# Kernel tuning notes

Measured on AMD Instinct MI355X. Metric: run time of the kernel, lower is better.

The kernel has to match this reference:

```python
import jax, jax.numpy as jnp
import numpy as np

NUM_HEADS = 8
LN_EPS = 1e-5


def layer_norm(x, g, b):
    m = jnp.mean(x, axis=-1, keepdims=True)
    v = jnp.mean((x - m) ** 2, axis=-1, keepdims=True)
    return (x - m) * jax.lax.rsqrt(v + LN_EPS) * g + b


def setup_inputs() -> dict:
    key = jax.random.key(0)
    B, Nq, Nk, D = 4, 2048, 2048, 256
    F = 4 * D
    ks = jax.random.split(key, 12)
    s = 0.02
    inp = {
        "q": jax.random.normal(ks[0], (B, Nq, D), jnp.float32),
        "x": jax.random.normal(ks[1], (B, Nk, D), jnp.float32),
        "Wq": jax.random.normal(ks[2], (D, D), jnp.float32) * s,
        "bq": jnp.zeros((D,), jnp.float32),
        "Wk": jax.random.normal(ks[3], (D, D), jnp.float32) * s,
        "bk": jnp.zeros((D,), jnp.float32),
        "Wv": jax.random.normal(ks[4], (D, D), jnp.float32) * s,
        "bv": jnp.zeros((D,), jnp.float32),
        "Wo": jax.random.normal(ks[5], (D, D), jnp.float32) * s,
        "bo": jnp.zeros((D,), jnp.float32),
        "Wm": jax.random.normal(ks[6], (D, F), jnp.float32) * s,
        "bm": jnp.zeros((F,), jnp.float32),
        "We": jax.random.normal(ks[7], (F, D), jnp.float32) * s,
        "be": jnp.zeros((D,), jnp.float32),
        "g0": jnp.ones((D,), jnp.float32),
        "b0": jnp.zeros((D,), jnp.float32),
        "g1": jnp.ones((D,), jnp.float32),
        "b1": jnp.zeros((D,), jnp.float32),
    }
    return inp


def reference(q, x, Wq, bq, Wk, bk, Wv, bv, Wo, bo, Wm, bm, We, be, g0, b0, g1, b1):
    B, Nq, D = q.shape
    H = NUM_HEADS
    dh = D // H
    scale = 1.0 / np.sqrt(dh).astype(np.float32)
    # projections, split into heads (split(dim_split,2)+cat(.,0) == head reshape)
    Q = (q @ Wq + bq).reshape(B, Nq, H, dh)
    K = (x @ Wk + bk).reshape(B, -1, H, dh)
    V = (x @ Wv + bv).reshape(B, -1, H, dh)
    A = jax.nn.softmax(jnp.einsum("bqhd,bkhd->bhqk", Q, K) * scale, axis=-1)
    # residual on the projected query (Q_ + A @ V_), merge heads
    O = (Q + jnp.einsum("bhqk,bkhd->bqhd", A, V)).reshape(B, Nq, D)
    O = layer_norm(O, g0, b0)
    O = O + jax.nn.relu(O @ Wo + bo)
    identity = O
    O = layer_norm(O, g1, b1)  # dropout p=0.0 is identity
    O = jax.nn.relu(O @ Wm + bm) @ We + be
    return O + identity
```

## Files before the change

kernel.cpp:

```cpp
#include <hip/hip_runtime.h>
#include <math.h>
#include <stdint.h>

typedef __attribute__((ext_vector_type(8))) __bf16 bf16x8;
typedef __attribute__((ext_vector_type(16))) float f32x16;

#define Z16 {0.f,0.f,0.f,0.f,0.f,0.f,0.f,0.f,0.f,0.f,0.f,0.f,0.f,0.f,0.f,0.f}

__device__ __forceinline__ unsigned short f2b(float f) {
  union { float f; uint32_t u; } v; v.f = f;
  uint32_t r = (v.u + 0x7FFFu + ((v.u >> 16) & 1u)) >> 16;
  return (unsigned short)r;
}
__device__ __forceinline__ float b2f(unsigned short u) {
  union { uint32_t u; float f; } v; v.u = ((uint32_t)u) << 16;
  return v.f;
}
__device__ __forceinline__ uint32_t pk2(float a, float b) {
  return (uint32_t)f2b(a) | ((uint32_t)f2b(b) << 16);
}
__device__ __forceinline__ uint32_t cvtpk(float lo, float hi) {
  uint32_t r;
  asm("v_cvt_pk_bf16_f32 %0, %1, %2" : "=v"(r) : "v"(lo), "v"(hi));
  return r;
}
__device__ __forceinline__ void glds16(const void* g, void* l) {
  __builtin_amdgcn_global_load_lds(
      (const __attribute__((address_space(1))) void*)g,
      (__attribute__((address_space(3))) void*)l, 16, 0, 0);
}
#define MFMA32(a, b, c) __builtin_amdgcn_mfma_f32_32x32x16_bf16(a, b, c, 0, 0, 0)

__global__ __launch_bounds__(256) void prep(
    const float* __restrict__ q, const float* __restrict__ x,
    unsigned short* __restrict__ qh, unsigned short* __restrict__ xh,
    const float* __restrict__ Wq, const float* __restrict__ Wk,
    const float* __restrict__ Wv, const float* __restrict__ Wo,
    const float* __restrict__ Wm, const float* __restrict__ We,
    unsigned short* __restrict__ WqT, unsigned short* __restrict__ WkvT,
    unsigned short* __restrict__ WoT, unsigned short* __restrict__ WmT,
    unsigned short* __restrict__ WeT,
    const float* __restrict__ bk, const float* __restrict__ bv,
    float* __restrict__ bkv) {
  __shared__ float T[64][68];
  const int bx = blockIdx.x, tid = threadIdx.x;
  if (bx < 2048) {
    const float* src = (bx < 1024) ? q : x;
    unsigned short* dst = (bx < 1024) ? qh : xh;
    const int i = (bx & 1023) * 256 + tid;
    float4 a = ((const float4*)src)[i * 2];
    float4 b = ((const float4*)src)[i * 2 + 1];
    uint4 o;
    o.x = cvtpk(a.x, a.y); o.y = cvtpk(a.z, a.w);
    o.z = cvtpk(b.x, b.y); o.w = cvtpk(b.z, b.w);
    ((uint4*)dst)[i] = o;
  } else if (bx < 2240) {
    int t = bx - 2048;
    const float* in; unsigned short* out; int ldin, ldout, kx, nx;
    if (t < 16)       { in = Wq; out = WqT;           ldin = 256;  ldout = 256;  kx = t & 3;  nx = t >> 2; }
    else if (t < 32)  { t -= 16;  in = Wk; out = WkvT;          ldin = 256;  ldout = 256;  kx = t & 3;  nx = t >> 2; }
    else if (t < 48)  { t -= 32;  in = Wv; out = WkvT + 65536;  ldin = 256;  ldout = 256;  kx = t & 3;  nx = t >> 2; }
    else if (t < 64)  { t -= 48;  in = Wo; out = WoT;           ldin = 256;  ldout = 256;  kx = t & 3;  nx = t >> 2; }
    else if (t < 128) { t -= 64;  in = Wm; out = WmT;           ldin = 1024; ldout = 256;  kx = t & 3;  nx = t >> 2; }
    else              { t -= 128; in = We; out = WeT;           ldin = 256;  ldout = 1024; kx = t & 15; nx = t >> 4; }
    const int k0 = kx * 64, n0 = nx * 64;
    const int r = tid >> 2, c16 = (tid & 3) * 16;
    #pragma unroll
    for (int i = 0; i < 4; ++i)
      *(float4*)&T[r][c16 + i * 4] =
          *(const float4*)&in[(size_t)(k0 + r) * ldin + n0 + c16 + i * 4];
    __syncthreads();
    const int n = tid >> 2, k16 = (tid & 3) * 16;
    uint32_t wb[8];
    #pragma unroll
    for (int p = 0; p < 8; ++p)
      wb[p] = cvtpk(T[k16 + 2 * p][n], T[k16 + 2 * p + 1][n]);
    uint4 o0, o1;
    o0.x = wb[0]; o0.y = wb[1]; o0.z = wb[2]; o0.w = wb[3];
    o1.x = wb[4]; o1.y = wb[5]; o1.z = wb[6]; o1.w = wb[7];
    *(uint4*)&out[(size_t)(n0 + n) * ldout + k0 + k16] = o0;
    *(uint4*)&out[(size_t)(n0 + n) * ldout + k0 + k16 + 8] = o1;
  } else {
    if (tid < 256) { bkv[tid] = bk[tid]; bkv[256 + tid] = bv[tid]; }
  }
}

__global__ __launch_bounds__(256, 2) void gemm_kv(
    const unsigned short* __restrict__ A, int lda,
    const unsigned short* __restrict__ Bt, int ldb,
    const float* __restrict__ bias,
    unsigned short* __restrict__ VtOut,
    void* __restrict__ Cout, int ldc, int K) {
  __shared__ __align__(16) unsigned short As[2 * 128 * 64];
  __shared__ __align__(16) unsigned short Bs[2 * 64 * 64];
  const int tid = threadIdx.x, lane = tid & 63, wid = tid >> 6;
  const int l31 = lane & 31, g2 = lane >> 5;
  const int m0 = blockIdx.x * 128, n0 = blockIdx.y * 64;

  const char* srcA[4];
  const char* srcB[2];
  #pragma unroll
  for (int p = 0; p < 4; ++p) {
    int row = p * 32 + wid * 8 + (lane >> 3);
    srcA[p] = (const char*)A + ((size_t)(m0 + row) * lda) * 2 + (lane & 7) * 16;
  }
  #pragma unroll
  for (int p = 0; p < 2; ++p) {
    int row = p * 32 + wid * 8 + (lane >> 3);
    srcB[p] = (const char*)Bt + ((size_t)(n0 + row) * ldb) * 2 + (lane & 7) * 16;
  }

  f32x16 acc0 = Z16, acc1 = Z16;
  const int nt = K >> 6;

  #pragma unroll
  for (int p = 0; p < 4; ++p) { glds16(srcA[p], &As[p * 2048 + wid * 512]); srcA[p] += 128; }
  #pragma unroll
  for (int p = 0; p < 2; ++p) { glds16(srcB[p], &Bs[p * 2048 + wid * 512]); srcB[p] += 128; }
  __syncthreads();

  for (int t = 0; t < nt; ++t) {
    const int cur = t & 1, nxt = cur ^ 1;
    if (t + 1 < nt) {
      #pragma unroll
      for (int p = 0; p < 4; ++p) { glds16(srcA[p], &As[nxt * 8192 + p * 2048 + wid * 512]); srcA[p] += 128; }
      #pragma unroll
      for (int p = 0; p < 2; ++p) { glds16(srcB[p], &Bs[nxt * 4096 + p * 2048 + wid * 512]); srcB[p] += 128; }
    }
    const char* as = (const char*)As + cur * 16384;
    const char* bs = (const char*)Bs + cur * 8192;
    #pragma unroll
    for (int kc = 0; kc < 4; ++kc) {
      const int xo = kc * 32 + g2 * 16;
      bf16x8 af  = *(const bf16x8*)(as + (wid * 32 + l31) * 128 + xo);
      bf16x8 b0v = *(const bf16x8*)(bs + l31 * 128 + xo);
      bf16x8 b1v = *(const bf16x8*)(bs + (32 + l31) * 128 + xo);
      acc0 = MFMA32(af, b0v, acc0);
      acc1 = MFMA32(af, b1v, acc1);
    }
    __syncthreads();
  }

  const int bb = m0 >> 11;
  #pragma unroll
  for (int nb = 0; nb < 2; ++nb) {
    const f32x16& acc = nb ? acc1 : acc0;
    const int col = n0 + nb * 32 + l31;
    const float bs = bias[col];
    if (n0 < 256) {
      #pragma unroll
      for (int r = 0; r < 16; ++r) {
        const int m = m0 + wid * 32 + (r & 3) + 8 * (r >> 2) + 4 * g2;
        ((unsigned short*)Cout)[(size_t)m * ldc + col] = f2b(acc[r] + bs);
      }
    } else {
      const int hv = (col - 256) >> 5, dv = (col - 256) & 31;
      unsigned short* vrow = VtOut + ((size_t)(bb * 8 + hv) * 32 + dv) * 2048;
      #pragma unroll
      for (int tq = 0; tq < 4; ++tq) {
        const int ks = (m0 & 2047) + wid * 32 + 8 * tq + 4 * g2;
        uint2 wv;
        wv.x = pk2(acc[4 * tq + 0] + bs, acc[4 * tq + 1] + bs);
        wv.y = pk2(acc[4 * tq + 2] + bs, acc[4 * tq + 3] + bs);
        *(uint2*)(vrow + ks) = wv;
      }
    }
  }
}

template <int EPI>
__global__ __launch_bounds__(256, 2) void gemm_small(
    const unsigned short* __restrict__ A, int lda,
    const unsigned short* __restrict__ Bt, int ldb,
    const float* __restrict__ bias,
    const unsigned short* __restrict__ res, int ldr,
    void* __restrict__ Cout, int ldc, int K) {
  __shared__ __align__(16) unsigned short As[2 * 64 * 64];
  __shared__ __align__(16) unsigned short Bs[2 * 64 * 64];
  const int tid = threadIdx.x, lane = tid & 63, wid = tid >> 6;
  const int l31 = lane & 31, g2 = lane >> 5;
  const int m0 = blockIdx.x * 64, n0 = blockIdx.y * 64;
  const int wr = (wid >> 1) * 32, wc = (wid & 1) * 32;

  const char* srcA[2];
  const char* srcB[2];
  #pragma unroll
  for (int p = 0; p < 2; ++p) {
    int row = p * 32 + wid * 8 + (lane >> 3);
    srcA[p] = (const char*)A + ((size_t)(m0 + row) * lda) * 2 + (lane & 7) * 16;
    srcB[p] = (const char*)Bt + ((size_t)(n0 + row) * ldb) * 2 + (lane & 7) * 16;
  }

  f32x16 acc = Z16;
  const int nt = K >> 6;

  #pragma unroll
  for (int p = 0; p < 2; ++p) {
    glds16(srcA[p], &As[p * 2048 + wid * 512]); srcA[p] += 128;
    glds16(srcB[p], &Bs[p * 2048 + wid * 512]); srcB[p] += 128;
  }
  __syncthreads();

  for (int t = 0; t < nt; ++t) {
    const int cur = t & 1, nxt = cur ^ 1;
    if (t + 1 < nt) {
      #pragma unroll
      for (int p = 0; p < 2; ++p) {
        glds16(srcA[p], &As[nxt * 4096 + p * 2048 + wid * 512]); srcA[p] += 128;
        glds16(srcB[p], &Bs[nxt * 4096 + p * 2048 + wid * 512]); srcB[p] += 128;
      }
    }
    const char* as = (const char*)As + cur * 8192;
    const char* bs = (const char*)Bs + cur * 8192;
    #pragma unroll
    for (int kc = 0; kc < 4; ++kc) {
      const int xo = kc * 32 + g2 * 16;
      bf16x8 af = *(const bf16x8*)(as + (wr + l31) * 128 + xo);
      bf16x8 bf = *(const bf16x8*)(bs + (wc + l31) * 128 + xo);
      acc = MFMA32(af, bf, acc);
    }
    __syncthreads();
  }

  const int col = n0 + wc + l31;
  const float bs = bias[col];
  #pragma unroll
  for (int r = 0; r < 16; ++r) {
    const int m = m0 + wr + (r & 3) + 8 * (r >> 2) + 4 * g2;
    float v = acc[r] + bs;
    if (EPI == 1) v = fmaxf(v, 0.f);
    if (EPI == 1 || EPI == 3) v += b2f(res[(size_t)m * ldr + col]);
    if (EPI == 3)
      ((float*)Cout)[(size_t)m * ldc + col] = v;
    else
      ((unsigned short*)Cout)[(size_t)m * ldc + col] = f2b(v);
  }
}

__global__ __launch_bounds__(256, 2) void gemm_relu128(
    const unsigned short* __restrict__ A, int lda,
    const unsigned short* __restrict__ Bt, int ldb,
    const float* __restrict__ bias,
    unsigned short* __restrict__ Cout, int ldc, int K) {
  __shared__ __align__(16) unsigned short As[2 * 128 * 64];
  __shared__ __align__(16) unsigned short Bs[2 * 128 * 64];
  const int tid = threadIdx.x, lane = tid & 63, wid = tid >> 6;
  const int l31 = lane & 31, g2 = lane >> 5;
  const int m0 = blockIdx.x * 128, n0 = blockIdx.y * 128;
  const int wr = (wid >> 1) * 64, wc = (wid & 1) * 64;

  const char* srcA[4];
  const char* srcB[4];
  #pragma unroll
  for (int p = 0; p < 4; ++p) {
    int row = p * 32 + wid * 8 + (lane >> 3);
    srcA[p] = (const char*)A + ((size_t)(m0 + row) * lda) * 2 + (lane & 7) * 16;
    srcB[p] = (const char*)Bt + ((size_t)(n0 + row) * ldb) * 2 + (lane & 7) * 16;
  }

  f32x16 a00 = Z16, a01 = Z16, a10 = Z16, a11 = Z16;
  const int nt = K >> 6;

  #pragma unroll
  for (int p = 0; p < 4; ++p) {
    glds16(srcA[p], &As[p * 2048 + wid * 512]); srcA[p] += 128;
    glds16(srcB[p], &Bs[p * 2048 + wid * 512]); srcB[p] += 128;
  }
  __syncthreads();

  for (int t = 0; t < nt; ++t) {
    const int cur = t & 1, nxt = cur ^ 1;
    if (t + 1 < nt) {
      #pragma unroll
      for (int p = 0; p < 4; ++p) {
        glds16(srcA[p], &As[nxt * 8192 + p * 2048 + wid * 512]); srcA[p] += 128;
        glds16(srcB[p], &Bs[nxt * 8192 + p * 2048 + wid * 512]); srcB[p] += 128;
      }
    }
    const char* as = (const char*)As + cur * 16384;
    const char* bs = (const char*)Bs + cur * 16384;
    #pragma unroll
    for (int kc = 0; kc < 4; ++kc) {
      const int xo = kc * 32 + g2 * 16;
      bf16x8 af0 = *(const bf16x8*)(as + (wr + l31) * 128 + xo);
      bf16x8 af1 = *(const bf16x8*)(as + (wr + 32 + l31) * 128 + xo);
      bf16x8 bf0 = *(const bf16x8*)(bs + (wc + l31) * 128 + xo);
      bf16x8 bf1 = *(const bf16x8*)(bs + (wc + 32 + l31) * 128 + xo);
      a00 = MFMA32(af0, bf0, a00);
      a01 = MFMA32(af0, bf1, a01);
      a10 = MFMA32(af1, bf0, a10);
      a11 = MFMA32(af1, bf1, a11);
    }
    __syncthreads();
  }

  #pragma unroll
  for (int mf = 0; mf < 2; ++mf)
    #pragma unroll
    for (int nb = 0; nb < 2; ++nb) {
      const f32x16& acc = mf ? (nb ? a11 : a10) : (nb ? a01 : a00);
      const int col = n0 + wc + nb * 32 + l31;
      const float bs = bias[col];
      #pragma unroll
      for (int r = 0; r < 16; ++r) {
        const int m = m0 + wr + mf * 32 + (r & 3) + 8 * (r >> 2) + 4 * g2;
        Cout[(size_t)m * ldc + col] = f2b(fmaxf(acc[r] + bs, 0.f));
      }
    }
}

#define KLD 40
#define VLD 72
__global__ __launch_bounds__(256, 4) void attn4(
    const unsigned short* __restrict__ Qg,
    const unsigned short* __restrict__ Kb,
    const unsigned short* __restrict__ Vt,
    float* __restrict__ Op0, float* __restrict__ Op1,
    unsigned short* __restrict__ lp) {
  __shared__ __align__(16) unsigned short Ks[64 * KLD];
  __shared__ __align__(16) unsigned short Vs[32 * VLD];
  const int tid = threadIdx.x, lane = tid & 63, wid = tid >> 6;
  const int l31 = lane & 31, g2 = lane >> 5;
  const int w = (blockIdx.x >> 3) + (blockIdx.x & 7) * 128;
  const int b = w >> 8, h = (w >> 5) & 7, kv = (w >> 4) & 1, qt = w & 15;
  const int row0 = b * 2048 + qt * 128;
  const int qrow = row0 + wid * 32 + l31;
  const int kt0 = kv * 1024;

  const float SCL2 = 0.17677669529663687f * 1.4426950408889634f;
  bf16x8 qf0, qf1;
  {
    const unsigned short* qp = Qg + (size_t)qrow * 256 + h * 32 + g2 * 8;
    #pragma unroll
    for (int dc = 0; dc < 2; ++dc) {
      ushort4 r0 = *(const ushort4*)(qp + dc * 16);
      ushort4 r1 = *(const ushort4*)(qp + dc * 16 + 4);
      union { unsigned short s[8]; bf16x8 v; } u;
      u.s[0] = f2b(b2f(r0.x) * SCL2); u.s[1] = f2b(b2f(r0.y) * SCL2);
      u.s[2] = f2b(b2f(r0.z) * SCL2); u.s[3] = f2b(b2f(r0.w) * SCL2);
      u.s[4] = f2b(b2f(r1.x) * SCL2); u.s[5] = f2b(b2f(r1.y) * SCL2);
      u.s[6] = f2b(b2f(r1.z) * SCL2); u.s[7] = f2b(b2f(r1.w) * SCL2);
      if (dc == 0) qf0 = u.v; else qf1 = u.v;
    }
  }

  const int ksr = tid >> 2, ksc = (tid & 3) * 8;
  const unsigned short* srcK = Kb + (size_t)(b * 2048 + kt0 + ksr) * 256 + h * 32 + ksc;
  const int vd = tid >> 3, vk = (tid & 7) * 8;
  const unsigned short* srcV = Vt + ((size_t)((b * 8 + h) * 32 + vd)) * 2048 + kt0 + vk;

  uint4 kreg = *(const uint4*)srcK;
  uint4 vreg = *(const uint4*)srcV;

  f32x16 oacc = Z16;
  float lr0 = 0.f, lr1 = 0.f;

  for (int kt = 0; kt < 1024; kt += 64) {
    *(uint4*)&Ks[ksr * KLD + ksc] = kreg;
    *(uint4*)&Vs[vd * VLD + vk] = vreg;
    __syncthreads();

    if (kt + 64 < 1024) {
      srcK += 64 * 256;
      kreg = *(const uint4*)srcK;
      srcV += 64;
      vreg = *(const uint4*)srcV;
    }

    f32x16 p0 = Z16, p1 = Z16;
    {
      bf16x8 k00 = *(const bf16x8*)&Ks[l31 * KLD + g2 * 8];
      bf16x8 k01 = *(const bf16x8*)&Ks[l31 * KLD + 16 + g2 * 8];
      bf16x8 k10 = *(const bf16x8*)&Ks[(32 + l31) * KLD + g2 * 8];
      bf16x8 k11 = *(const bf16x8*)&Ks[(32 + l31) * KLD + 16 + g2 * 8];
      p0 = MFMA32(k00, qf0, p0);
      p0 = MFMA32(k01, qf1, p0);
      p1 = MFMA32(k10, qf0, p1);
      p1 = MFMA32(k11, qf1, p1);
    }

    float s0 = 0.f, s1 = 0.f;
    #pragma unroll
    for (int i = 0; i < 16; ++i) { p0[i] = __builtin_amdgcn_exp2f(p0[i]); s0 += p0[i]; }
    #pragma unroll
    for (int i = 0; i < 16; ++i) { p1[i] = __builtin_amdgcn_exp2f(p1[i]); s1 += p1[i]; }
    lr0 += s0; lr1 += s1;

    #pragma unroll
    for (int rb = 0; rb < 2; ++rb) {
      const f32x16& pp = rb ? p1 : p0;
      #pragma unroll
      for (int c = 0; c < 2; ++c) {
        uint32_t A0 = cvtpk(pp[8 * c + 0], pp[8 * c + 1]);
        uint32_t A1 = cvtpk(pp[8 * c + 2], pp[8 * c + 3]);
        uint32_t B0 = cvtpk(pp[8 * c + 4], pp[8 * c + 5]);
        uint32_t B1 = cvtpk(pp[8 * c + 6], pp[8 * c + 7]);
        uint32_t pA0 = (uint32_t)__shfl_xor((int)A0, 32);
        uint32_t pB0 = (uint32_t)__shfl_xor((int)B0, 32);
        uint32_t pA1 = (uint32_t)__shfl_xor((int)A1, 32);
        uint32_t pB1 = (uint32_t)__shfl_xor((int)B1, 32);
        union { uint32_t u[4]; bf16x8 v; } fr;
        fr.u[0] = g2 ? pB0 : A0;
        fr.u[1] = g2 ? pB1 : A1;
        fr.u[2] = g2 ? B0 : pA0;
        fr.u[3] = g2 ? B1 : pA1;
        bf16x8 vf = *(const bf16x8*)&Vs[l31 * VLD + rb * 32 + c * 16 + g2 * 8];
        oacc = MFMA32(vf, fr.v, oacc);
      }
    }
    __syncthreads();
  }

  float lrun = lr0 + lr1;
  lrun += __shfl_xor(lrun, 32);
  float* op = (kv ? Op1 : Op0) + (size_t)qrow * 256 + h * 32;
  #pragma unroll
  for (int j = 0; j < 4; ++j) {
    float4 v = make_float4(oacc[4 * j + 0], oacc[4 * j + 1],
                           oacc[4 * j + 2], oacc[4 * j + 3]);
    *(float4*)(op + 8 * j + 4 * g2) = v;
  }
  if (g2 == 0)
    lp[(((size_t)kv * 4 + b) * 8 + h) * 2048 + (qt * 128 + wid * 32 + l31)] = f2b(lrun);
}

__global__ __launch_bounds__(256) void combine_ln0(
    const float* __restrict__ Op0, const float* __restrict__ Op1,
    const unsigned short* __restrict__ lp,
    const unsigned short* __restrict__ Qb,
    const float* __restrict__ gw, const float* __restrict__ bw,
    unsigned short* __restrict__ O1n) {
  const int wid = threadIdx.x >> 6, lane = threadIdx.x & 63;
  const int row = blockIdx.x * 4 + wid;
  const int b = row >> 11, rr = row & 2047, hh = lane >> 3;
  const float la = b2f(lp[(((size_t)0 * 4 + b) * 8 + hh) * 2048 + rr]);
  const float lb = b2f(lp[(((size_t)1 * 4 + b) * 8 + hh) * 2048 + rr]);
  const float inv = 1.f / (la + lb);
  float4 oa = *(const float4*)&Op0[(size_t)row * 256 + lane * 4];
  float4 ob = *(const float4*)&Op1[(size_t)row * 256 + lane * 4];
  ushort4 qv = *(const ushort4*)(Qb + (size_t)row * 256 + lane * 4);
  float x0 = b2f(qv.x) + (oa.x + ob.x) * inv;
  float x1 = b2f(qv.y) + (oa.y + ob.y) * inv;
  float x2 = b2f(qv.z) + (oa.z + ob.z) * inv;
  float x3 = b2f(qv.w) + (oa.w + ob.w) * inv;
  float s = x0 + x1 + x2 + x3;
  float sq = x0 * x0 + x1 * x1 + x2 * x2 + x3 * x3;
  #pragma unroll
  for (int off = 32; off >= 1; off >>= 1) {
    s += __shfl_xor(s, off);
    sq += __shfl_xor(sq, off);
  }
  const float mean = s * (1.f / 256.f);
  const float var = sq * (1.f / 256.f) - mean * mean;
  const float rstd = rsqrtf(var + 1e-5f);
  float4 gv = *(const float4*)&gw[lane * 4];
  float4 bv = *(const float4*)&bw[lane * 4];
  ushort4 o;
  o.x = f2b((x0 - mean) * rstd * gv.x + bv.x);
  o.y = f2b((x1 - mean) * rstd * gv.y + bv.y);
  o.z = f2b((x2 - mean) * rstd * gv.z + bv.z);
  o.w = f2b((x3 - mean) * rstd * gv.w + bv.w);
  *(ushort4*)(O1n + (size_t)row * 256 + lane * 4) = o;
}

__global__ __launch_bounds__(256) void ln_k(
    const unsigned short* __restrict__ X, const float* __restrict__ gw,
    const float* __restrict__ bw, unsigned short* __restrict__ Y) {
  const int wid = threadIdx.x >> 6, lane = threadIdx.x & 63;
  const int row = blockIdx.x * 4 + wid;
  ushort4 xv = *(const ushort4*)(X + (size_t)row * 256 + lane * 4);
  float x0 = b2f(xv.x), x1 = b2f(xv.y), x2 = b2f(xv.z), x3 = b2f(xv.w);
  float s = x0 + x1 + x2 + x3;
  float sq = x0 * x0 + x1 * x1 + x2 * x2 + x3 * x3;
  #pragma unroll
  for (int off = 32; off >= 1; off >>= 1) {
    s += __shfl_xor(s, off);
    sq += __shfl_xor(sq, off);
  }
  const float mean = s * (1.f / 256.f);
  const float var = sq * (1.f / 256.f) - mean * mean;
  const float rstd = rsqrtf(var + 1e-5f);
  float4 gv = *(const float4*)&gw[lane * 4];
  float4 bv = *(const float4*)&bw[lane * 4];
  ushort4 o;
  o.x = f2b((x0 - mean) * rstd * gv.x + bv.x);
  o.y = f2b((x1 - mean) * rstd * gv.y + bv.y);
  o.z = f2b((x2 - mean) * rstd * gv.z + bv.z);
  o.w = f2b((x3 - mean) * rstd * gv.w + bv.w);
  *(ushort4*)(Y + (size_t)row * 256 + lane * 4) = o;
}

extern "C" void kernel_launch(void* const* d_in, const int* in_sizes, int n_in,
                              void* d_out, int out_size, void* d_ws, size_t ws_size,
                              hipStream_t stream) {
  (void)in_sizes; (void)n_in; (void)out_size; (void)ws_size;
  const float* q = (const float*)d_in[0];
  const float* x = (const float*)d_in[1];
  const float* Wq = (const float*)d_in[2];
  const float* bq = (const float*)d_in[3];
  const float* Wk = (const float*)d_in[4];
  const float* bk = (const float*)d_in[5];
  const float* Wv = (const float*)d_in[6];
  const float* bv = (const float*)d_in[7];
  const float* Wo = (const float*)d_in[8];
  const float* bo = (const float*)d_in[9];
  const float* Wm = (const float*)d_in[10];
  const float* bm = (const float*)d_in[11];
  const float* We = (const float*)d_in[12];
  const float* be = (const float*)d_in[13];
  const float* g0 = (const float*)d_in[14];
  const float* b0 = (const float*)d_in[15];
  const float* g1 = (const float*)d_in[16];
  const float* b1 = (const float*)d_in[17];
  float* out = (float*)d_out;

  uint8_t* ws = (uint8_t*)d_ws;
  unsigned short* WqT  = (unsigned short*)(ws + 0);
  unsigned short* WkvT = (unsigned short*)(ws + 131072);
  unsigned short* WoT  = (unsigned short*)(ws + 393216);
  unsigned short* WmT  = (unsigned short*)(ws + 524288);
  unsigned short* WeT  = (unsigned short*)(ws + 1048576);
  float*          bkv  = (float*)(ws + 1572864);
  unsigned short* qh   = (unsigned short*)(ws + 1576960);
  unsigned short* xh   = (unsigned short*)(ws + 5771264);
  unsigned short* Qb   = (unsigned short*)(ws + 9965568);
  unsigned short* Kb   = (unsigned short*)(ws + 14159872);
  unsigned short* Vt   = (unsigned short*)(ws + 18354176);
  unsigned short* lpart = (unsigned short*)(ws + 0);
  float* Op1 = (float*)(ws + 1576960);
  float* Op0 = (float*)(ws + 22548480);
  unsigned short* O1n = (unsigned short*)(ws + 14159872);
  unsigned short* O2  = (unsigned short*)(ws + 1576960);
  unsigned short* O2n = (unsigned short*)(ws + 5771264);
  unsigned short* Mb  = (unsigned short*)(ws + 14159872);

  prep<<<2241, 256, 0, stream>>>(q, x, qh, xh, Wq, Wk, Wv, Wo, Wm, We,
                                 WqT, WkvT, WoT, WmT, WeT, bk, bv, bkv);

  gemm_small<0><<<dim3(128, 4), 256, 0, stream>>>(qh, 256, WqT, 256, bq, nullptr, 0, Qb, 256, 256);
  gemm_kv<<<dim3(64, 8), 256, 0, stream>>>(xh, 256, WkvT, 256, bkv, Vt, Kb, 256, 256);

  attn4<<<1024, 256, 0, stream>>>(Qb, Kb, Vt, Op0, Op1, lpart);
  combine_ln0<<<2048, 256, 0, stream>>>(Op0, Op1, lpart, Qb, g0, b0, O1n);

  gemm_small<1><<<dim3(128, 4), 256, 0, stream>>>(O1n, 256, WoT, 256, bo, O1n, 256, O2, 256, 256);
  ln_k<<<2048, 256, 0, stream>>>(O2, g1, b1, O2n);

  gemm_relu128<<<dim3(64, 8), 256, 0, stream>>>(O2n, 256, WmT, 256, bm, Mb, 1024, 256);
  gemm_small<3><<<dim3(128, 4), 256, 0, stream>>>(Mb, 1024, WeT, 1024, be, O2, 256, out, 256, 1024);
}
```

Measured before the change: 117.6 us.

## Fuse Q and KV projections, split attention KV four ways with bf16 partials

```diff
diff --git a/kernel.cpp b/kernel.cpp
--- a/kernel.cpp
+++ b/kernel.cpp
@@ -85,33 +85,37 @@
   }
 }
 
-__global__ __launch_bounds__(256, 2) void gemm_kv(
-    const unsigned short* __restrict__ A, int lda,
-    const unsigned short* __restrict__ Bt, int ldb,
-    const float* __restrict__ bias,
-    unsigned short* __restrict__ VtOut,
-    void* __restrict__ Cout, int ldc, int K) {
+__global__ __launch_bounds__(256, 2) void gemm_proj(
+    const unsigned short* __restrict__ qh, const unsigned short* __restrict__ xh,
+    const unsigned short* __restrict__ WqT, const unsigned short* __restrict__ WkvT,
+    const float* __restrict__ bq, const float* __restrict__ bkv,
+    unsigned short* __restrict__ Qb, unsigned short* __restrict__ Kb,
+    unsigned short* __restrict__ Vt) {
   __shared__ __align__(16) unsigned short As[2 * 128 * 64];
   __shared__ __align__(16) unsigned short Bs[2 * 64 * 64];
   const int tid = threadIdx.x, lane = tid & 63, wid = tid >> 6;
   const int l31 = lane & 31, g2 = lane >> 5;
-  const int m0 = blockIdx.x * 128, n0 = blockIdx.y * 64;
+  const bool qmode = blockIdx.y < 4;
+  const int m0 = blockIdx.x * 128;
+  const int n0 = qmode ? blockIdx.y * 64 : (blockIdx.y - 4) * 64;
+  const unsigned short* A = qmode ? qh : xh;
+  const unsigned short* Bt = qmode ? WqT : WkvT;
+  const float* bias = qmode ? bq : bkv;
 
   const char* srcA[4];
   const char* srcB[2];
   #pragma unroll
   for (int p = 0; p < 4; ++p) {
     int row = p * 32 + wid * 8 + (lane >> 3);
-    srcA[p] = (const char*)A + ((size_t)(m0 + row) * lda) * 2 + (lane & 7) * 16;
+    srcA[p] = (const char*)A + ((size_t)(m0 + row) * 256) * 2 + (lane & 7) * 16;
   }
   #pragma unroll
   for (int p = 0; p < 2; ++p) {
     int row = p * 32 + wid * 8 + (lane >> 3);
-    srcB[p] = (const char*)Bt + ((size_t)(n0 + row) * ldb) * 2 + (lane & 7) * 16;
+    srcB[p] = (const char*)Bt + ((size_t)(n0 + row) * 256) * 2 + (lane & 7) * 16;
   }
 
   f32x16 acc0 = Z16, acc1 = Z16;
-  const int nt = K >> 6;
 
   #pragma unroll
   for (int p = 0; p < 4; ++p) { glds16(srcA[p], &As[p * 2048 + wid * 512]); srcA[p] += 128; }
@@ -119,9 +123,9 @@
   for (int p = 0; p < 2; ++p) { glds16(srcB[p], &Bs[p * 2048 + wid * 512]); srcB[p] += 128; }
   __syncthreads();
 
-  for (int t = 0; t < nt; ++t) {
+  for (int t = 0; t < 4; ++t) {
     const int cur = t & 1, nxt = cur ^ 1;
-    if (t + 1 < nt) {
+    if (t + 1 < 4) {
       #pragma unroll
       for (int p = 0; p < 4; ++p) { glds16(srcA[p], &As[nxt * 8192 + p * 2048 + wid * 512]); srcA[p] += 128; }
       #pragma unroll
@@ -147,15 +151,21 @@
     const f32x16& acc = nb ? acc1 : acc0;
     const int col = n0 + nb * 32 + l31;
     const float bs = bias[col];
-    if (n0 < 256) {
+    if (qmode) {
       #pragma unroll
       for (int r = 0; r < 16; ++r) {
         const int m = m0 + wid * 32 + (r & 3) + 8 * (r >> 2) + 4 * g2;
-        ((unsigned short*)Cout)[(size_t)m * ldc + col] = f2b(acc[r] + bs);
+        Qb[(size_t)m * 256 + col] = f2b(acc[r] + bs);
+      }
+    } else if (n0 < 256) {
+      #pragma unroll
+      for (int r = 0; r < 16; ++r) {
+        const int m = m0 + wid * 32 + (r & 3) + 8 * (r >> 2) + 4 * g2;
+        Kb[(size_t)m * 256 + col] = f2b(acc[r] + bs);
       }
     } else {
       const int hv = (col - 256) >> 5, dv = (col - 256) & 31;
-      unsigned short* vrow = VtOut + ((size_t)(bb * 8 + hv) * 32 + dv) * 2048;
+      unsigned short* vrow = Vt + ((size_t)(bb * 8 + hv) * 32 + dv) * 2048;
       #pragma unroll
       for (int tq = 0; tq < 4; ++tq) {
         const int ks = (m0 & 2047) + wid * 32 + 8 * tq + 4 * g2;
@@ -311,21 +321,22 @@
 
 #define KLD 40
 #define VLD 72
-__global__ __launch_bounds__(256, 4) void attn4(
+__global__ __launch_bounds__(256, 8) void attn5(
     const unsigned short* __restrict__ Qg,
     const unsigned short* __restrict__ Kb,
     const unsigned short* __restrict__ Vt,
-    float* __restrict__ Op0, float* __restrict__ Op1,
+    unsigned short* __restrict__ Op0, unsigned short* __restrict__ Op1,
+    unsigned short* __restrict__ Op2, unsigned short* __restrict__ Op3,
     unsigned short* __restrict__ lp) {
   __shared__ __align__(16) unsigned short Ks[64 * KLD];
   __shared__ __align__(16) unsigned short Vs[32 * VLD];
   const int tid = threadIdx.x, lane = tid & 63, wid = tid >> 6;
   const int l31 = lane & 31, g2 = lane >> 5;
-  const int w = (blockIdx.x >> 3) + (blockIdx.x & 7) * 128;
-  const int b = w >> 8, h = (w >> 5) & 7, kv = (w >> 4) & 1, qt = w & 15;
+  const int w = (blockIdx.x >> 3) + (blockIdx.x & 7) * 256;
+  const int b = w >> 9, h = (w >> 6) & 7, kv = (w >> 4) & 3, qt = w & 15;
   const int row0 = b * 2048 + qt * 128;
   const int qrow = row0 + wid * 32 + l31;
-  const int kt0 = kv * 1024;
+  const int kt0 = kv * 512;
 
   const float SCL2 = 0.17677669529663687f * 1.4426950408889634f;
   bf16x8 qf0, qf1;
@@ -355,12 +366,12 @@
   f32x16 oacc = Z16;
   float lr0 = 0.f, lr1 = 0.f;
 
-  for (int kt = 0; kt < 1024; kt += 64) {
+  for (int kt = 0; kt < 512; kt += 64) {
     *(uint4*)&Ks[ksr * KLD + ksc] = kreg;
     *(uint4*)&Vs[vd * VLD + vk] = vreg;
     __syncthreads();
 
-    if (kt + 64 < 1024) {
+    if (kt + 64 < 512) {
       srcK += 64 * 256;
       kreg = *(const uint4*)srcK;
       srcV += 64;
@@ -413,19 +424,23 @@
 
   float lrun = lr0 + lr1;
   lrun += __shfl_xor(lrun, 32);
-  float* op = (kv ? Op1 : Op0) + (size_t)qrow * 256 + h * 32;
+  unsigned short* op =
+      (kv == 0 ? Op0 : kv == 1 ? Op1 : kv == 2 ? Op2 : Op3) +
+      (size_t)qrow * 256 + h * 32;
   #pragma unroll
   for (int j = 0; j < 4; ++j) {
-    float4 v = make_float4(oacc[4 * j + 0], oacc[4 * j + 1],
-                           oacc[4 * j + 2], oacc[4 * j + 3]);
-    *(float4*)(op + 8 * j + 4 * g2) = v;
+    uint2 wv;
+    wv.x = cvtpk(oacc[4 * j + 0], oacc[4 * j + 1]);
+    wv.y = cvtpk(oacc[4 * j + 2], oacc[4 * j + 3]);
+    *(uint2*)(op + 8 * j + 4 * g2) = wv;
   }
   if (g2 == 0)
     lp[(((size_t)kv * 4 + b) * 8 + h) * 2048 + (qt * 128 + wid * 32 + l31)] = f2b(lrun);
 }
 
 __global__ __launch_bounds__(256) void combine_ln0(
-    const float* __restrict__ Op0, const float* __restrict__ Op1,
+    const unsigned short* __restrict__ Op0, const unsigned short* __restrict__ Op1,
+    const unsigned short* __restrict__ Op2, const unsigned short* __restrict__ Op3,
     const unsigned short* __restrict__ lp,
     const unsigned short* __restrict__ Qb,
     const float* __restrict__ gw, const float* __restrict__ bw,
@@ -433,22 +448,27 @@
   const int wid = threadIdx.x >> 6, lane = threadIdx.x & 63;
   const int row = blockIdx.x * 4 + wid;
   const int b = row >> 11, rr = row & 2047, hh = lane >> 3;
-  const float la = b2f(lp[(((size_t)0 * 4 + b) * 8 + hh) * 2048 + rr]);
-  const float lb = b2f(lp[(((size_t)1 * 4 + b) * 8 + hh) * 2048 + rr]);
-  const float inv = 1.f / (la + lb);
-  float4 oa = *(const float4*)&Op0[(size_t)row * 256 + lane * 4];
-  float4 ob = *(const float4*)&Op1[(size_t)row * 256 + lane * 4];
-  ushort4 qv = *(const ushort4*)(Qb + (size_t)row * 256 + lane * 4);
-  float x0 = b2f(qv.x) + (oa.x + ob.x) * inv;
-  float x1 = b2f(qv.y) + (oa.y + ob.y) * inv;
-  float x2 = b2f(qv.z) + (oa.z + ob.z) * inv;
-  float x3 = b2f(qv.w) + (oa.w + ob.w) * inv;
+  float lsum = 0.f;
+  #pragma unroll
+  for (int s = 0; s < 4; ++s)
+    lsum += b2f(lp[(((size_t)s * 4 + b) * 8 + hh) * 2048 + rr]);
+  const float inv = 1.f / lsum;
+  const size_t off = (size_t)row * 256 + lane * 4;
+  ushort4 oa = *(const ushort4*)(Op0 + off);
+  ushort4 ob = *(const ushort4*)(Op1 + off);
+  ushort4 oc = *(const ushort4*)(Op2 + off);
+  ushort4 od = *(const ushort4*)(Op3 + off);
+  ushort4 qv = *(const ushort4*)(Qb + off);
+  float x0 = b2f(qv.x) + (b2f(oa.x) + b2f(ob.x) + b2f(oc.x) + b2f(od.x)) * inv;
+  float x1 = b2f(qv.y) + (b2f(oa.y) + b2f(ob.y) + b2f(oc.y) + b2f(od.y)) * inv;
+  float x2 = b2f(qv.z) + (b2f(oa.z) + b2f(ob.z) + b2f(oc.z) + b2f(od.z)) * inv;
+  float x3 = b2f(qv.w) + (b2f(oa.w) + b2f(ob.w) + b2f(oc.w) + b2f(od.w)) * inv;
   float s = x0 + x1 + x2 + x3;
   float sq = x0 * x0 + x1 * x1 + x2 * x2 + x3 * x3;
   #pragma unroll
-  for (int off = 32; off >= 1; off >>= 1) {
-    s += __shfl_xor(s, off);
-    sq += __shfl_xor(sq, off);
+  for (int off2 = 32; off2 >= 1; off2 >>= 1) {
+    s += __shfl_xor(s, off2);
+    sq += __shfl_xor(sq, off2);
   }
   const float mean = s * (1.f / 256.f);
   const float var = sq * (1.f / 256.f) - mean * mean;
@@ -460,7 +480,7 @@
   o.y = f2b((x1 - mean) * rstd * gv.y + bv.y);
   o.z = f2b((x2 - mean) * rstd * gv.z + bv.z);
   o.w = f2b((x3 - mean) * rstd * gv.w + bv.w);
-  *(ushort4*)(O1n + (size_t)row * 256 + lane * 4) = o;
+  *(ushort4*)(O1n + off) = o;
 }
 
 __global__ __launch_bounds__(256) void ln_k(
@@ -515,20 +535,22 @@
   float* out = (float*)d_out;
 
   uint8_t* ws = (uint8_t*)d_ws;
-  unsigned short* WqT  = (unsigned short*)(ws + 0);
-  unsigned short* WkvT = (unsigned short*)(ws + 131072);
-  unsigned short* WoT  = (unsigned short*)(ws + 393216);
-  unsigned short* WmT  = (unsigned short*)(ws + 524288);
-  unsigned short* WeT  = (unsigned short*)(ws + 1048576);
-  float*          bkv  = (float*)(ws + 1572864);
+  unsigned short* WoT  = (unsigned short*)(ws + 0);
+  unsigned short* WmT  = (unsigned short*)(ws + 131072);
+  unsigned short* WeT  = (unsigned short*)(ws + 655360);
+  float*          bkv  = (float*)(ws + 1179648);
+  unsigned short* WqT  = (unsigned short*)(ws + 1181696);
+  unsigned short* WkvT = (unsigned short*)(ws + 1312768);
   unsigned short* qh   = (unsigned short*)(ws + 1576960);
   unsigned short* xh   = (unsigned short*)(ws + 5771264);
   unsigned short* Qb   = (unsigned short*)(ws + 9965568);
   unsigned short* Kb   = (unsigned short*)(ws + 14159872);
   unsigned short* Vt   = (unsigned short*)(ws + 18354176);
-  unsigned short* lpart = (unsigned short*)(ws + 0);
-  float* Op1 = (float*)(ws + 1576960);
-  float* Op0 = (float*)(ws + 22548480);
+  unsigned short* lp   = (unsigned short*)(ws + 22548480);
+  unsigned short* Op0 = qh;
+  unsigned short* Op1 = xh;
+  unsigned short* Op2 = (unsigned short*)d_out;
+  unsigned short* Op3 = (unsigned short*)d_out + 2097152;
   unsigned short* O1n = (unsigned short*)(ws + 14159872);
   unsigned short* O2  = (unsigned short*)(ws + 1576960);
   unsigned short* O2n = (unsigned short*)(ws + 5771264);
@@ -537,11 +559,10 @@
   prep<<<2241, 256, 0, stream>>>(q, x, qh, xh, Wq, Wk, Wv, Wo, Wm, We,
                                  WqT, WkvT, WoT, WmT, WeT, bk, bv, bkv);
 
-  gemm_small<0><<<dim3(128, 4), 256, 0, stream>>>(qh, 256, WqT, 256, bq, nullptr, 0, Qb, 256, 256);
-  gemm_kv<<<dim3(64, 8), 256, 0, stream>>>(xh, 256, WkvT, 256, bkv, Vt, Kb, 256, 256);
-
-  attn4<<<1024, 256, 0, stream>>>(Qb, Kb, Vt, Op0, Op1, lpart);
-  combine_ln0<<<2048, 256, 0, stream>>>(Op0, Op1, lpart, Qb, g0, b0, O1n);
+  gemm_proj<<<dim3(64, 12), 256, 0, stream>>>(qh, xh, WqT, WkvT, bq, bkv, Qb, Kb, Vt);
+
+  attn5<<<2048, 256, 0, stream>>>(Qb, Kb, Vt, Op0, Op1, Op2, Op3, lp);
+  combine_ln0<<<2048, 256, 0, stream>>>(Op0, Op1, Op2, Op3, lp, Qb, g0, b0, O1n);
 
   gemm_small<1><<<dim3(128, 4), 256, 0, stream>>>(O1n, 256, WoT, 256, bo, O1n, 256, O2, 256, 256);
   ln_k<<<2048, 256, 0, stream>>>(O2, g1, b1, O2n);
```

Measured after the change: 262.3 us. 2.23x slower.
